# Optimization experiments

Measured on AMD Instinct MI355X. Metric: run time of the kernel, lower is better.

Reference implementation:

```python
import jax, jax.numpy as jnp
import numpy as np

B, T, D = 2, 2048, 2048
H, KV = 16, 4
HD = D // H            # 128
N_REP = H // KV        # 4
KV_DIM = D * KV // H   # 512
ALIBI_W = 0.1


def _rotate_half(x):
    x1, x2 = jnp.split(x, 2, axis=-1)
    return jnp.concatenate([-x2, x1], axis=-1)


def _apply_rope(xq, xk, freqs_cis):
    # xq: [B,H,T,hd], xk: [B,KV,T,hd]; freqs_cis: [T, hd] (cos half | sin half)
    seq_len, head_dim = xq.shape[2], xq.shape[3]
    freqs = freqs_cis[:seq_len, :]
    half = head_dim // 2
    cos = jnp.repeat(freqs[:, :half], 2, axis=-1)[None, None]  # [1,1,T,hd]
    sin = jnp.repeat(freqs[:, half:], 2, axis=-1)[None, None]
    xq_out = xq * cos + _rotate_half(xq) * sin
    xk_out = xk * cos + _rotate_half(xk) * sin
    return xq_out, xk_out


def setup_inputs() -> dict:
    key = jax.random.key(0)
    ks = jax.random.split(key, 8)
    x = jax.random.normal(ks[0], (B, T, D), jnp.float32)
    # additive causal mask (0 on/below diag, -1e9 above)
    causal = jnp.tril(jnp.ones((T, T), jnp.bool_))
    mask = jnp.where(causal, 0.0, -1e9).astype(jnp.float32)[None, None]
    # RoPE table: first half cos, second half sin of t*theta
    inv_freq = 1.0 / (10000.0 ** (np.arange(0, HD, 2, dtype=np.float32) / HD))  # [hd/2]
    angles = jnp.arange(T, dtype=jnp.float32)[:, None] * jnp.asarray(inv_freq)[None, :]
    freqs_cis = jnp.concatenate([jnp.cos(angles), jnp.sin(angles)], axis=-1)  # [T, hd]
    # ALiBi bias: per-head slope * relative distance
    slopes = 2.0 ** (-8.0 * (jnp.arange(1, H + 1, dtype=jnp.float32) / H))  # [H]
    rel = (jnp.arange(T, dtype=jnp.float32)[None, :] - jnp.arange(T, dtype=jnp.float32)[:, None])
    alibi_bias = (-jnp.abs(rel)[None, None] * slopes[None, :, None, None]).astype(jnp.float32)
    std = 0.02
    Wq = std * jax.random.normal(ks[1], (D, D), jnp.float32)
    Wk = std * jax.random.normal(ks[2], (D, KV_DIM), jnp.float32)
    Wv = std * jax.random.normal(ks[3], (D, KV_DIM), jnp.float32)
    Wo = std * jax.random.normal(ks[4], (D, D), jnp.float32)
    return {"x": x, "mask": mask, "freqs_cis": freqs_cis, "alibi_bias": alibi_bias,
            "Wq": Wq, "Wk": Wk, "Wv": Wv, "Wo": Wo}


def reference(x, mask, freqs_cis, alibi_bias, Wq, Wk, Wv, Wo):
    b, t, d = x.shape
    q = (x @ Wq).reshape(b, t, H, HD).transpose(0, 2, 1, 3)      # [B,H,T,hd]
    k = (x @ Wk).reshape(b, t, KV, HD).transpose(0, 2, 1, 3)     # [B,KV,T,hd]
    v = (x @ Wv).reshape(b, t, KV, HD).transpose(0, 2, 1, 3)     # [B,KV,T,hd]
    q, k = _apply_rope(q, k, freqs_cis)
    # grouped-query scores: group query heads by kv head, avoid repeating K/V
    qg = q.reshape(b, KV, N_REP, t, HD)
    scores = jnp.einsum('bgrtd,bgsd->bgrts', qg, k) / jnp.sqrt(jnp.float32(HD))
    alibi = alibi_bias[:, :, :t, :t].reshape(1, KV, N_REP, t, t)
    scores = scores * (1.0 - ALIBI_W) + alibi * ALIBI_W
    scores = scores + mask[:, :, None, :t, :t]                   # broadcast [1,1,1,T,T]
    attn = jax.nn.softmax(scores.astype(jnp.float32), axis=-1).astype(x.dtype)
    out = jnp.einsum('bgrts,bgsd->bgrtd', attn, v)               # [B,KV,n_rep,T,hd]
    out = out.reshape(b, H, t, HD).transpose(0, 2, 1, 3).reshape(b, t, d)
    return out @ Wo
```

## Files before the change

### kernel.cpp

```cpp
#include <hip/hip_runtime.h>

#define T_SEQ 2048
#define D_MODEL 2048
#define NH 16
#define NKV 4
#define HEAD_DIM 128

typedef unsigned short u16;
typedef __attribute__((ext_vector_type(8))) short bf16x8;
typedef __attribute__((ext_vector_type(4))) float f32x4;

__device__ __forceinline__ float bf2f(u16 u) { return __uint_as_float(((unsigned)u) << 16); }
__device__ __forceinline__ u16 f2bf(float f) {
  unsigned x = __float_as_uint(f);
  return (u16)((x + 0x7FFFu + ((x >> 16) & 1u)) >> 16);
}
__device__ __forceinline__ float fexp2(float x) { return __builtin_amdgcn_exp2f(x); }

#define ASYNC_COPY16(g, l)                                                        \
  __builtin_amdgcn_global_load_lds((const __attribute__((address_space(1))) unsigned int*)(g), \
                                   (__attribute__((address_space(3))) unsigned int*)(l), 16, 0, 0)

#define BARRIER() do { asm volatile("" ::: "memory"); __builtin_amdgcn_s_barrier(); asm volatile("" ::: "memory"); } while (0)

template<int N> __device__ __forceinline__ void vmwait() {
  if constexpr (N == 0) asm volatile("s_waitcnt vmcnt(0)" ::: "memory");
  else if constexpr (N == 3) asm volatile("s_waitcnt vmcnt(3)" ::: "memory");
  else if constexpr (N == 4) asm volatile("s_waitcnt vmcnt(4)" ::: "memory");
  else if constexpr (N == 5) asm volatile("s_waitcnt vmcnt(5)" ::: "memory");
}

__global__ void cast_kernel(const float* __restrict__ x, u16* __restrict__ y, int n4) {
  int i = blockIdx.x * 256 + threadIdx.x;
  if (i >= n4) return;
  const float4 v = reinterpret_cast<const float4*>(x)[i];
  unsigned p0 = (unsigned)f2bf(v.x) | ((unsigned)f2bf(v.y) << 16);
  unsigned p1 = (unsigned)f2bf(v.z) | ((unsigned)f2bf(v.w) << 16);
  reinterpret_cast<uint2*>(y)[i] = make_uint2(p0, p1);
}

__global__ void transpose4_kernel(const float* __restrict__ Wq, const float* __restrict__ Wk,
                                  const float* __restrict__ Wv, const float* __restrict__ Wo,
                                  u16* __restrict__ qkvT, u16* __restrict__ WoT) {
  __shared__ float t[32][33];
  const int m = blockIdx.z;
  const float* W; u16* WT; int N;
  if (m == 0)      { W = Wq; WT = qkvT;                         N = 2048; }
  else if (m == 1) { W = Wk; WT = qkvT + (size_t)2048 * 2048;   N = 512;  }
  else if (m == 2) { W = Wv; WT = qkvT + (size_t)2560 * 2048;   N = 512;  }
  else             { W = Wo; WT = WoT;                          N = 2048; }
  const int n0 = blockIdx.x * 32, k0 = blockIdx.y * 32;
  if (n0 >= N) return;
  const int tx = threadIdx.x, ty = threadIdx.y;
#pragma unroll
  for (int i = 0; i < 32; i += 8)
    t[ty + i][tx] = W[(size_t)(k0 + ty + i) * N + n0 + tx];
  __syncthreads();
#pragma unroll
  for (int i = 0; i < 32; i += 8)
    WT[(size_t)(n0 + ty + i) * 2048 + k0 + tx] = f2bf(t[tx][ty + i]);
}

template<int BM, int BN, int WM, int WN, int EA, int EB, int OUT_BF16, int WRITE_VT>
__global__ __launch_bounds__(512, 1) void gemm_dp(const u16* __restrict__ A, const u16* __restrict__ BT,
                                                  void* __restrict__ Cv, u16* __restrict__ vt_out,
                                                  int M, int N, int K, int nbx) {
  constexpr int PA = BM / 64, PB = BN / 64;
  constexpr int E = EA + EB;
  constexpr int FM = BM / WM / 16, FN = BN / WN / 16;
  static_assert(FM % 2 == 0 && FN % 2 == 0, "quadrant split");
  __shared__ u16 SA[2][BM * 64];
  __shared__ u16 SB[2][BN * 64];
  const int tid = threadIdx.x;
  const int wave = tid >> 6, lane = tid & 63;
  const int lr = lane & 15, lg = lane >> 4;
  const int wm = wave / WN, wn = wave % WN;
  const int nwg = gridDim.x;
  const int bid = blockIdx.x;
  const int swz = (bid & 7) * (nwg >> 3) + (bid >> 3);
  const int bx = swz % nbx, by = swz / nbx;
  const size_t arow0 = (size_t)by * BM;
  const size_t brow0 = (size_t)bx * BN;
  const int NT = K >> 6;

  const int srow = tid >> 3;
  const int scol = ((tid & 7) ^ (srow & 7)) << 3;

  f32x4 acc[FM][FN] = {};
  bf16x8 af[FM / 2][2], bf0[FN / 2][2], bf1[FN / 2][2];

  const u16* Abase = A + arow0 * K;
  const u16* Bbase = BT + brow0 * K;

  auto stageA = [&](int p, int ktile, int buf) {
    if (ktile >= NT) return;
    const u16* src = Abase + (size_t)(p * 64 + srow) * K + (ktile << 6) + scol;
    ASYNC_COPY16(src, &SA[buf][(p * 64 + wave * 8) * 64]);
  };
  auto stageB = [&](int p, int ktile, int buf) {
    if (ktile >= NT) return;
    const u16* src = Bbase + (size_t)(p * 64 + srow) * K + (ktile << 6) + scol;
    ASYNC_COPY16(src, &SB[buf][(p * 64 + wave * 8) * 64]);
  };
  auto ldA = [&](int c, int mh) {
#pragma unroll
    for (int mf = 0; mf < FM / 2; ++mf)
#pragma unroll
      for (int ks = 0; ks < 2; ++ks) {
        const int row = wm * (BM / WM) + (mh * (FM / 2) + mf) * 16 + lr;
        const int slot = ((ks << 2) | lg) ^ (lr & 7);
        af[mf][ks] = *reinterpret_cast<const bf16x8*>(&SA[c][row * 64 + (slot << 3)]);
      }
  };
  auto ldB = [&](int c, int nh, bf16x8 (*bfr)[2]) {
#pragma unroll
    for (int nf = 0; nf < FN / 2; ++nf)
#pragma unroll
      for (int ks = 0; ks < 2; ++ks) {
        const int row = wn * (BN / WN) + (nh * (FN / 2) + nf) * 16 + lr;
        const int slot = ((ks << 2) | lg) ^ (lr & 7);
        bfr[nf][ks] = *reinterpret_cast<const bf16x8*>(&SB[c][row * 64 + (slot << 3)]);
      }
  };
  auto mq = [&](int mh, int nh, bf16x8 (*bfr)[2]) {
    __builtin_amdgcn_s_setprio(1);
#pragma unroll
    for (int mf = 0; mf < FM / 2; ++mf)
#pragma unroll
      for (int nf = 0; nf < FN / 2; ++nf)
#pragma unroll
        for (int ks = 0; ks < 2; ++ks)
          acc[mh * (FM / 2) + mf][nh * (FN / 2) + nf] = __builtin_amdgcn_mfma_f32_16x16x32_bf16(
              af[mf][ks], bfr[nf][ks], acc[mh * (FM / 2) + mf][nh * (FN / 2) + nf], 0, 0, 0);
    __builtin_amdgcn_s_setprio(0);
  };

#pragma unroll
  for (int p = 0; p < PA; ++p) stageA(p, 0, 0);
#pragma unroll
  for (int p = 0; p < PB; ++p) stageB(p, 0, 0);
#pragma unroll
  for (int p = 0; p < EB; ++p) stageB(p, 1, 1);
#pragma unroll
  for (int p = 0; p < EA; ++p) stageA(p, 1, 1);
  vmwait<E>();
  BARRIER();

  for (int kt = 0; kt < NT; ++kt) {
    const int c = kt & 1;
    ldA(c, 0); ldB(c, 0, bf0);
#pragma unroll
    for (int p = EB; p < PB; ++p) stageB(p, kt + 1, c ^ 1);
    BARRIER();
    mq(0, 0, bf0);
    BARRIER();
    ldB(c, 1, bf1);
#pragma unroll
    for (int p = EA; p < PA; ++p) stageA(p, kt + 1, c ^ 1);
    BARRIER();
    mq(0, 1, bf1);
    BARRIER();
    ldA(c, 1);
#pragma unroll
    for (int p = 0; p < EB; ++p) stageB(p, kt + 2, c);
    BARRIER();
    mq(1, 1, bf1);
    BARRIER();
#pragma unroll
    for (int p = 0; p < EA; ++p) stageA(p, kt + 2, c);
    BARRIER();
    mq(1, 0, bf0);
    if (kt + 2 < NT) vmwait<E>(); else vmwait<0>();
    BARRIER();
  }

#pragma unroll
  for (int mf = 0; mf < FM; ++mf)
#pragma unroll
    for (int nf = 0; nf < FN; ++nf) {
      const size_t col = brow0 + wn * (BN / WN) + nf * 16 + lr;
      const size_t row0 = arow0 + wm * (BM / WM) + mf * 16 + lg * 4;
      if (WRITE_VT && col >= 2560) {
        const int bb = (int)(row0 >> 11);
        const int t0 = (int)(row0 & 2047);
        u16 tmp[4];
#pragma unroll
        for (int r = 0; r < 4; ++r) tmp[r] = f2bf(acc[mf][nf][r]);
        *reinterpret_cast<uint2*>(vt_out + ((size_t)(bb * 512 + (int)(col - 2560))) * 2048 + t0) =
            *reinterpret_cast<const uint2*>(tmp);
      } else {
#pragma unroll
        for (int r = 0; r < 4; ++r) {
          const size_t row = row0 + r;
          if (OUT_BF16) ((u16*)Cv)[row * N + col] = f2bf(acc[mf][nf][r]);
          else          ((float*)Cv)[row * N + col] = acc[mf][nf][r];
        }
      }
    }
}

__global__ void ropek_kernel(u16* __restrict__ qkv, const float* __restrict__ freqs) {
  int idx = blockIdx.x * 256 + threadIdx.x;
  u16* p = qkv + 2048;
  int d = idx & 63;
  int h = (idx >> 6) & 3;
  int row = idx >> 8;
  int t = row & (T_SEQ - 1);
  size_t base = (size_t)row * 3072 + (size_t)h * 128;
  float x1 = bf2f(p[base + d]);
  float x2 = bf2f(p[base + 64 + d]);
  const float* fr = freqs + (size_t)t * 128;
  int dh = d >> 1;
  float c1 = fr[dh],      s1 = fr[64 + dh];
  float c2 = fr[32 + dh], s2 = fr[96 + dh];
  p[base + d]      = f2bf(x1 * c1 - x2 * s1);
  p[base + 64 + d] = f2bf(x2 * c2 + x1 * s2);
}

__global__ __launch_bounds__(512) void attn_kernel(const u16* __restrict__ q, const u16* __restrict__ k,
                                                   const u16* __restrict__ vt, u16* __restrict__ o,
                                                   const float* __restrict__ freqs,
                                                   int qstride, int kstride) {
  __shared__ u16 Kl[2][64][136];
  __shared__ u16 Vl[2][128][72];
  __shared__ u16 Pl[8][16][72];
  const int b = blockIdx.z, h = blockIdx.y, pairIdx = blockIdx.x;
  const int g = h >> 2;
  const int tid = threadIdx.x, wave = tid >> 6, lane = tid & 63;
  const int lr = lane & 15, lg = lane >> 4;

  const float LOG2E = 1.44269504089f;
  const float qk_scale = 0.9f / sqrtf(128.f) * LOG2E;
  const float slope2   = 0.1f * fexp2(-0.5f * (h + 1)) * LOG2E;
  const float THR = 16.0f;

  const int krow = tid >> 3, kc0 = (tid & 7) * 16;
  const int vrow = tid >> 2, vc0 = (tid & 3) * 16;
  const u16* kbp = k + ((size_t)(b * T_SEQ + krow)) * kstride + g * HEAD_DIM + kc0;
  const u16* vbp = vt + ((size_t)((b * NKV + g) * HEAD_DIM + vrow)) * T_SEQ + vc0;

  float cb[4];
#pragma unroll
  for (int nt = 0; nt < 4; ++nt) cb[nt] = slope2 * (float)(nt * 16 + lr);

  for (int half = 0; half < 2; ++half) {
    const int qt = half ? (15 - pairIdx) : pairIdx;
    const int qbase = qt * 128;
    const int trow = qbase + wave * 16 + lr;

    const u16* qp = q + ((size_t)(b * T_SEQ + trow)) * qstride + h * HEAD_DIM;
    bf16x8 qf[4];
#pragma unroll
    for (int ks = 0; ks < 4; ++ks) qf[ks] = *reinterpret_cast<const bf16x8*>(qp + ks * 32 + lg * 8);
    {
      const float* frq = freqs + (size_t)trow * 128;
#pragma unroll
      for (int ks = 0; ks < 2; ++ks)
#pragma unroll
        for (int j = 0; j < 8; ++j) {
          const int dh = (ks * 32 + lg * 8 + j) >> 1;
          float x1 = bf2f((u16)qf[ks][j]);
          float x2 = bf2f((u16)qf[ks + 2][j]);
          qf[ks][j]     = (short)f2bf(x1 * frq[dh]      - x2 * frq[64 + dh]);
          qf[ks + 2][j] = (short)f2bf(x2 * frq[32 + dh] + x1 * frq[96 + dh]);
        }
    }

    f32x4 oa[8] = {};
    float m_r[4], l_r[4];
#pragma unroll
    for (int r = 0; r < 4; ++r) { m_r[r] = -1e30f; l_r[r] = 0.f; }

    const int ktmax = 2 * qt + 1;
    const int irow_min_w = qbase + wave * 16;
    const int irow_max_w = irow_min_w + 15;
    int cur = 0;

    __syncthreads();
    {
      bf16x8 k0a = *reinterpret_cast<const bf16x8*>(kbp);
      bf16x8 k0b = *reinterpret_cast<const bf16x8*>(kbp + 8);
      bf16x8 v0a = *reinterpret_cast<const bf16x8*>(vbp);
      bf16x8 v0b = *reinterpret_cast<const bf16x8*>(vbp + 8);
      *reinterpret_cast<bf16x8*>(&Kl[0][krow][kc0]) = k0a;
      *reinterpret_cast<bf16x8*>(&Kl[0][krow][kc0 + 8]) = k0b;
      *reinterpret_cast<bf16x8*>(&Vl[0][vrow][vc0]) = v0a;
      *reinterpret_cast<bf16x8*>(&Vl[0][vrow][vc0 + 8]) = v0b;
    }

    for (int kt = 0; kt <= ktmax; ++kt) {
      const int kbase = kt * 64;
      __syncthreads();

      const bool pf = (kt < ktmax);
      bf16x8 pk0, pk1, pv0, pv1;
      if (pf) {
        const u16* ks2p = kbp + (size_t)(kbase + 64) * kstride;
        pk0 = *reinterpret_cast<const bf16x8*>(ks2p);
        pk1 = *reinterpret_cast<const bf16x8*>(ks2p + 8);
        const u16* vs2p = vbp + kbase + 64;
        pv0 = *reinterpret_cast<const bf16x8*>(vs2p);
        pv1 = *reinterpret_cast<const bf16x8*>(vs2p + 8);
      }

      const bool compute = (kbase <= irow_max_w);
      if (compute) {
        f32x4 sa[4] = {};
#pragma unroll
        for (int nt = 0; nt < 4; ++nt)
#pragma unroll
          for (int ks = 0; ks < 4; ++ks)
            sa[nt] = __builtin_amdgcn_mfma_f32_16x16x32_bf16(
                qf[ks], *reinterpret_cast<const bf16x8*>(&Kl[cur][nt * 16 + lr][ks * 32 + lg * 8]), sa[nt], 0, 0, 0);

        const int i_row0 = irow_min_w + lg * 4;
        const float tb = slope2 * (float)kbase;
        float sv[4][4];
        float pmx[4] = {-1e30f, -1e30f, -1e30f, -1e30f};
        if (kbase + 63 <= irow_min_w) {
#pragma unroll
          for (int nt = 0; nt < 4; ++nt) {
            const float bias = cb[nt] + tb;
#pragma unroll
            for (int r = 0; r < 4; ++r) {
              float xv = fmaf(sa[nt][r], qk_scale, bias);
              sv[nt][r] = xv;
              pmx[r] = fmaxf(pmx[r], xv);
            }
          }
        } else {
#pragma unroll
          for (int nt = 0; nt < 4; ++nt) {
            const int jcol = kbase + nt * 16 + lr;
            const float bias = cb[nt] + tb;
#pragma unroll
            for (int r = 0; r < 4; ++r) {
              float xv = (jcol <= i_row0 + r) ? fmaf(sa[nt][r], qk_scale, bias) : -1e30f;
              sv[nt][r] = xv;
              pmx[r] = fmaxf(pmx[r], xv);
            }
          }
        }

        bool okl = true;
#pragma unroll
        for (int r = 0; r < 4; ++r) okl = okl && (pmx[r] <= m_r[r] + THR);
        if (__all(okl)) {
          float rs[4] = {0.f, 0.f, 0.f, 0.f};
#pragma unroll
          for (int nt = 0; nt < 4; ++nt)
#pragma unroll
            for (int r = 0; r < 4; ++r) {
              float p = fexp2(sv[nt][r] - m_r[r]);
              sv[nt][r] = p;
              rs[r] += p;
            }
#pragma unroll
          for (int r = 0; r < 4; ++r) l_r[r] += rs[r];
        } else {
#pragma unroll
          for (int mm = 1; mm < 16; mm <<= 1)
#pragma unroll
            for (int r = 0; r < 4; ++r) pmx[r] = fmaxf(pmx[r], __shfl_xor(pmx[r], mm, 64));
          float corr[4], rs[4];
#pragma unroll
          for (int r = 0; r < 4; ++r) {
            float mn = fmaxf(m_r[r], pmx[r]);
            corr[r] = fexp2(m_r[r] - mn);
            m_r[r] = mn;
            rs[r] = 0.f;
          }
#pragma unroll
          for (int nt = 0; nt < 4; ++nt)
#pragma unroll
            for (int r = 0; r < 4; ++r) {
              float p = fexp2(sv[nt][r] - m_r[r]);
              sv[nt][r] = p;
              rs[r] += p;
            }
#pragma unroll
          for (int r = 0; r < 4; ++r) l_r[r] = l_r[r] * corr[r] + rs[r];
#pragma unroll
          for (int t8 = 0; t8 < 8; ++t8)
#pragma unroll
            for (int r = 0; r < 4; ++r) oa[t8][r] *= corr[r];
        }

#pragma unroll
        for (int nt = 0; nt < 4; ++nt)
#pragma unroll
          for (int r = 0; r < 4; ++r)
            Pl[wave][lg * 4 + r][nt * 16 + lr] = f2bf(sv[nt][r]);
      }

      if (pf) {
        *reinterpret_cast<bf16x8*>(&Kl[cur ^ 1][krow][kc0]) = pk0;
        *reinterpret_cast<bf16x8*>(&Kl[cur ^ 1][krow][kc0 + 8]) = pk1;
        *reinterpret_cast<bf16x8*>(&Vl[cur ^ 1][vrow][vc0]) = pv0;
        *reinterpret_cast<bf16x8*>(&Vl[cur ^ 1][vrow][vc0 + 8]) = pv1;
      }

      if (compute) {
#pragma unroll
        for (int ht = 0; ht < 8; ++ht)
#pragma unroll
          for (int ks2 = 0; ks2 < 2; ++ks2) {
            bf16x8 pa = *reinterpret_cast<const bf16x8*>(&Pl[wave][lr][ks2 * 32 + lg * 8]);
            bf16x8 vb8 = *reinterpret_cast<const bf16x8*>(&Vl[cur][ht * 16 + lr][ks2 * 32 + lg * 8]);
            oa[ht] = __builtin_amdgcn_mfma_f32_16x16x32_bf16(pa, vb8, oa[ht], 0, 0, 0);
          }
      }
      cur ^= 1;
    }

#pragma unroll
    for (int mm = 1; mm < 16; mm <<= 1)
#pragma unroll
      for (int r = 0; r < 4; ++r) l_r[r] += __shfl_xor(l_r[r], mm, 64);

    u16* op = o + ((size_t)(b * T_SEQ + qbase + wave * 16)) * D_MODEL + h * HEAD_DIM;
#pragma unroll
    for (int r = 0; r < 4; ++r) {
      float inv = 1.0f / l_r[r];
#pragma unroll
      for (int ht = 0; ht < 8; ++ht)
        op[(size_t)(lg * 4 + r) * D_MODEL + ht * 16 + lr] = f2bf(oa[ht][r] * inv);
    }
  }
}

extern "C" void kernel_launch(void* const* d_in, const int* in_sizes, int n_in,
                              void* d_out, int out_size, void* d_ws, size_t ws_size,
                              hipStream_t stream) {
  (void)in_sizes; (void)n_in; (void)out_size; (void)ws_size;
  const float* x     = (const float*)d_in[0];
  const float* freqs = (const float*)d_in[2];
  const float* Wq    = (const float*)d_in[4];
  const float* Wk    = (const float*)d_in[5];
  const float* Wv    = (const float*)d_in[6];
  const float* Wo    = (const float*)d_in[7];
  float* out = (float*)d_out;
  char* ws = (char*)d_ws;
  const size_t MB = 1024 * 1024;
  u16* xb   = (u16*)(ws);
  u16* qkvT = (u16*)(ws + 16 * MB);
  u16* WoT  = (u16*)(ws + 28 * MB);
  u16* qkv  = (u16*)(ws + 36 * MB);
  u16* vtb  = (u16*)(ws + 60 * MB);
  const int M = 2 * T_SEQ;
  const int NQKV = 3072;

  cast_kernel<<<(M * D_MODEL / 4 + 255) / 256, 256, 0, stream>>>(x, xb, M * D_MODEL / 4);
  dim3 tb(32, 8);
  transpose4_kernel<<<dim3(64, 64, 4), tb, 0, stream>>>(Wq, Wk, Wv, Wo, qkvT, WoT);

  gemm_dp<256, 192, 4, 2, 2, 2, 1, 1><<<256, 512, 0, stream>>>(xb, qkvT, qkv, vtb, M, NQKV, 2048, NQKV / 192);

  ropek_kernel<<<(M * NKV * 64) / 256, 256, 0, stream>>>(qkv, freqs);

  attn_kernel<<<dim3(8, NH, 2), 512, 0, stream>>>(qkv, qkv + 2048, vtb, xb, freqs, NQKV, NQKV);

  gemm_dp<128, 256, 2, 4, 1, 2, 0, 0><<<256, 512, 0, stream>>>(xb, WoT, out, nullptr, M, 2048, 2048, 2048 / 256);
}
```

Measured before the change: 207.6 us.

## Load K/V fragments directly from global memory per wave, drop LDS staging

Removes the shared-memory double buffer for K and V and the block-wide barriers. Each wave now loads its MFMA operands directly from global memory and iterates only up to its own causal limit. This removes barrier synchronization and LDS traffic, but K/V reuse across the 8 waves now depends on cache hits, and global-load latency is no longer overlapped by prefetching.

```diff
diff --git a/kernel.cpp b/kernel.cpp
--- a/kernel.cpp
+++ b/kernel.cpp
@@ -221,8 +221,6 @@
                                                    const u16* __restrict__ vt, u16* __restrict__ o,
                                                    const float* __restrict__ freqs,
                                                    int qstride, int kstride) {
-  __shared__ u16 Kl[2][64][136];
-  __shared__ u16 Vl[2][128][72];
   __shared__ u16 Pl[8][16][72];
   const int b = blockIdx.z, h = blockIdx.y, pairIdx = blockIdx.x;
   const int g = h >> 2;
@@ -234,10 +232,8 @@
   const float slope2   = 0.1f * fexp2(-0.5f * (h + 1)) * LOG2E;
   const float THR = 16.0f;
 
-  const int krow = tid >> 3, kc0 = (tid & 7) * 16;
-  const int vrow = tid >> 2, vc0 = (tid & 3) * 16;
-  const u16* kbp = k + ((size_t)(b * T_SEQ + krow)) * kstride + g * HEAD_DIM + kc0;
-  const u16* vbp = vt + ((size_t)((b * NKV + g) * HEAD_DIM + vrow)) * T_SEQ + vc0;
+  const u16* kg = k + (size_t)(b * T_SEQ) * kstride + g * HEAD_DIM + lg * 8;
+  const u16* vg = vt + ((size_t)((b * NKV + g) * HEAD_DIM + lr)) * T_SEQ + lg * 8;
 
   float cb[4];
 #pragma unroll
@@ -271,146 +267,115 @@
 #pragma unroll
     for (int r = 0; r < 4; ++r) { m_r[r] = -1e30f; l_r[r] = 0.f; }
 
-    const int ktmax = 2 * qt + 1;
     const int irow_min_w = qbase + wave * 16;
     const int irow_max_w = irow_min_w + 15;
-    int cur = 0;
-
-    __syncthreads();
-    {
-      bf16x8 k0a = *reinterpret_cast<const bf16x8*>(kbp);
-      bf16x8 k0b = *reinterpret_cast<const bf16x8*>(kbp + 8);
-      bf16x8 v0a = *reinterpret_cast<const bf16x8*>(vbp);
-      bf16x8 v0b = *reinterpret_cast<const bf16x8*>(vbp + 8);
-      *reinterpret_cast<bf16x8*>(&Kl[0][krow][kc0]) = k0a;
-      *reinterpret_cast<bf16x8*>(&Kl[0][krow][kc0 + 8]) = k0b;
-      *reinterpret_cast<bf16x8*>(&Vl[0][vrow][vc0]) = v0a;
-      *reinterpret_cast<bf16x8*>(&Vl[0][vrow][vc0 + 8]) = v0b;
-    }
-
-    for (int kt = 0; kt <= ktmax; ++kt) {
+    const int ktmax_w = irow_max_w >> 6;
+
+    for (int kt = 0; kt <= ktmax_w; ++kt) {
       const int kbase = kt * 64;
-      __syncthreads();
-
-      const bool pf = (kt < ktmax);
-      bf16x8 pk0, pk1, pv0, pv1;
-      if (pf) {
-        const u16* ks2p = kbp + (size_t)(kbase + 64) * kstride;
-        pk0 = *reinterpret_cast<const bf16x8*>(ks2p);
-        pk1 = *reinterpret_cast<const bf16x8*>(ks2p + 8);
-        const u16* vs2p = vbp + kbase + 64;
-        pv0 = *reinterpret_cast<const bf16x8*>(vs2p);
-        pv1 = *reinterpret_cast<const bf16x8*>(vs2p + 8);
-      }
-
-      const bool compute = (kbase <= irow_max_w);
-      if (compute) {
-        f32x4 sa[4] = {};
+
+      f32x4 sa[4] = {};
+#pragma unroll
+      for (int nt = 0; nt < 4; ++nt) {
+        const u16* kp = kg + (size_t)(kbase + nt * 16 + lr) * kstride;
+#pragma unroll
+        for (int ks = 0; ks < 4; ++ks) {
+          bf16x8 kf = *reinterpret_cast<const bf16x8*>(kp + ks * 32);
+          sa[nt] = __builtin_amdgcn_mfma_f32_16x16x32_bf16(qf[ks], kf, sa[nt], 0, 0, 0);
+        }
+      }
+
+      const int i_row0 = irow_min_w + lg * 4;
+      const float tb = slope2 * (float)kbase;
+      float sv[4][4];
+      float pmx[4] = {-1e30f, -1e30f, -1e30f, -1e30f};
+      if (kbase + 63 <= irow_min_w) {
+#pragma unroll
+        for (int nt = 0; nt < 4; ++nt) {
+          const float bias = cb[nt] + tb;
+#pragma unroll
+          for (int r = 0; r < 4; ++r) {
+            float xv = fmaf(sa[nt][r], qk_scale, bias);
+            sv[nt][r] = xv;
+            pmx[r] = fmaxf(pmx[r], xv);
+          }
+        }
+      } else {
+#pragma unroll
+        for (int nt = 0; nt < 4; ++nt) {
+          const int jcol = kbase + nt * 16 + lr;
+          const float bias = cb[nt] + tb;
+#pragma unroll
+          for (int r = 0; r < 4; ++r) {
+            float xv = (jcol <= i_row0 + r) ? fmaf(sa[nt][r], qk_scale, bias) : -1e30f;
+            sv[nt][r] = xv;
+            pmx[r] = fmaxf(pmx[r], xv);
+          }
+        }
+      }
+
+      bool okl = true;
+#pragma unroll
+      for (int r = 0; r < 4; ++r) okl = okl && (pmx[r] <= m_r[r] + THR);
+      if (__all(okl)) {
+        float rs[4] = {0.f, 0.f, 0.f, 0.f};
 #pragma unroll
         for (int nt = 0; nt < 4; ++nt)
 #pragma unroll
-          for (int ks = 0; ks < 4; ++ks)
-            sa[nt] = __builtin_amdgcn_mfma_f32_16x16x32_bf16(
-                qf[ks], *reinterpret_cast<const bf16x8*>(&Kl[cur][nt * 16 + lr][ks * 32 + lg * 8]), sa[nt], 0, 0, 0);
-
-        const int i_row0 = irow_min_w + lg * 4;
-        const float tb = slope2 * (float)kbase;
-        float sv[4][4];
-        float pmx[4] = {-1e30f, -1e30f, -1e30f, -1e30f};
-        if (kbase + 63 <= irow_min_w) {
-#pragma unroll
-          for (int nt = 0; nt < 4; ++nt) {
-            const float bias = cb[nt] + tb;
-#pragma unroll
-            for (int r = 0; r < 4; ++r) {
-              float xv = fmaf(sa[nt][r], qk_scale, bias);
-              sv[nt][r] = xv;
-              pmx[r] = fmaxf(pmx[r], xv);
-            }
+          for (int r = 0; r < 4; ++r) {
+            float p = fexp2(sv[nt][r] - m_r[r]);
+            sv[nt][r] = p;
+            rs[r] += p;
           }
-        } else {
-#pragma unroll
-          for (int nt = 0; nt < 4; ++nt) {
-            const int jcol = kbase + nt * 16 + lr;
-            const float bias = cb[nt] + tb;
-#pragma unroll
-            for (int r = 0; r < 4; ++r) {
-              float xv = (jcol <= i_row0 + r) ? fmaf(sa[nt][r], qk_scale, bias) : -1e30f;
-              sv[nt][r] = xv;
-              pmx[r] = fmaxf(pmx[r], xv);
-            }
+#pragma unroll
+        for (int r = 0; r < 4; ++r) l_r[r] += rs[r];
+      } else {
+#pragma unroll
+        for (int mm = 1; mm < 16; mm <<= 1)
+#pragma unroll
+          for (int r = 0; r < 4; ++r) pmx[r] = fmaxf(pmx[r], __shfl_xor(pmx[r], mm, 64));
+        float corr[4], rs[4];
+#pragma unroll
+        for (int r = 0; r < 4; ++r) {
+          float mn = fmaxf(m_r[r], pmx[r]);
+          corr[r] = fexp2(m_r[r] - mn);
+          m_r[r] = mn;
+          rs[r] = 0.f;
+        }
+#pragma unroll
+        for (int nt = 0; nt < 4; ++nt)
+#pragma unroll
+          for (int r = 0; r < 4; ++r) {
+            float p = fexp2(sv[nt][r] - m_r[r]);
+            sv[nt][r] = p;
+            rs[r] += p;
           }
-        }
-
-        bool okl = true;
-#pragma unroll
-        for (int r = 0; r < 4; ++r) okl = okl && (pmx[r] <= m_r[r] + THR);
-        if (__all(okl)) {
-          float rs[4] = {0.f, 0.f, 0.f, 0.f};
-#pragma unroll
-          for (int nt = 0; nt < 4; ++nt)
-#pragma unroll
-            for (int r = 0; r < 4; ++r) {
-              float p = fexp2(sv[nt][r] - m_r[r]);
-              sv[nt][r] = p;
-              rs[r] += p;
-            }
-#pragma unroll
-          for (int r = 0; r < 4; ++r) l_r[r] += rs[r];
-        } else {
-#pragma unroll
-          for (int mm = 1; mm < 16; mm <<= 1)
-#pragma unroll
-            for (int r = 0; r < 4; ++r) pmx[r] = fmaxf(pmx[r], __shfl_xor(pmx[r], mm, 64));
-          float corr[4], rs[4];
-#pragma unroll
-          for (int r = 0; r < 4; ++r) {
-            float mn = fmaxf(m_r[r], pmx[r]);
-            corr[r] = fexp2(m_r[r] - mn);
-            m_r[r] = mn;
-            rs[r] = 0.f;
-          }
-#pragma unroll
-          for (int nt = 0; nt < 4; ++nt)
-#pragma unroll
-            for (int r = 0; r < 4; ++r) {
-              float p = fexp2(sv[nt][r] - m_r[r]);
-              sv[nt][r] = p;
-              rs[r] += p;
-            }
-#pragma unroll
-          for (int r = 0; r < 4; ++r) l_r[r] = l_r[r] * corr[r] + rs[r];
-#pragma unroll
-          for (int t8 = 0; t8 < 8; ++t8)
-#pragma unroll
-            for (int r = 0; r < 4; ++r) oa[t8][r] *= corr[r];
-        }
-
-#pragma unroll
-        for (int nt = 0; nt < 4; ++nt)
-#pragma unroll
-          for (int r = 0; r < 4; ++r)
-            Pl[wave][lg * 4 + r][nt * 16 + lr] = f2bf(sv[nt][r]);
-      }
-
-      if (pf) {
-        *reinterpret_cast<bf16x8*>(&Kl[cur ^ 1][krow][kc0]) = pk0;
-        *reinterpret_cast<bf16x8*>(&Kl[cur ^ 1][krow][kc0 + 8]) = pk1;
-        *reinterpret_cast<bf16x8*>(&Vl[cur ^ 1][vrow][vc0]) = pv0;
-        *reinterpret_cast<bf16x8*>(&Vl[cur ^ 1][vrow][vc0 + 8]) = pv1;
-      }
-
-      if (compute) {
-#pragma unroll
-        for (int ht = 0; ht < 8; ++ht)
-#pragma unroll
-          for (int ks2 = 0; ks2 < 2; ++ks2) {
-            bf16x8 pa = *reinterpret_cast<const bf16x8*>(&Pl[wave][lr][ks2 * 32 + lg * 8]);
-            bf16x8 vb8 = *reinterpret_cast<const bf16x8*>(&Vl[cur][ht * 16 + lr][ks2 * 32 + lg * 8]);
-            oa[ht] = __builtin_amdgcn_mfma_f32_16x16x32_bf16(pa, vb8, oa[ht], 0, 0, 0);
-          }
-      }
-      cur ^= 1;
+#pragma unroll
+        for (int r = 0; r < 4; ++r) l_r[r] = l_r[r] * corr[r] + rs[r];
+#pragma unroll
+        for (int t8 = 0; t8 < 8; ++t8)
+#pragma unroll
+          for (int r = 0; r < 4; ++r) oa[t8][r] *= corr[r];
+      }
+
+#pragma unroll
+      for (int nt = 0; nt < 4; ++nt)
+#pragma unroll
+        for (int r = 0; r < 4; ++r)
+          Pl[wave][lg * 4 + r][nt * 16 + lr] = f2bf(sv[nt][r]);
+
+      {
+        bf16x8 pa0 = *reinterpret_cast<const bf16x8*>(&Pl[wave][lr][lg * 8]);
+        bf16x8 pa1 = *reinterpret_cast<const bf16x8*>(&Pl[wave][lr][32 + lg * 8]);
+#pragma unroll
+        for (int ht = 0; ht < 8; ++ht) {
+          const u16* vp = vg + (size_t)(ht * 16) * T_SEQ + kbase;
+          bf16x8 vb0 = *reinterpret_cast<const bf16x8*>(vp);
+          oa[ht] = __builtin_amdgcn_mfma_f32_16x16x32_bf16(pa0, vb0, oa[ht], 0, 0, 0);
+          bf16x8 vb1 = *reinterpret_cast<const bf16x8*>(vp + 32);
+          oa[ht] = __builtin_amdgcn_mfma_f32_16x16x32_bf16(pa1, vb1, oa[ht], 0, 0, 0);
+        }
+      }
     }
 
 #pragma unroll
```

Measured after the change: 364.5 us. +75.6%, slower.
